# Kernel tuning notes

Hardware: AMD Instinct MI355X
Metric: run time of the kernel (lower is better)

## Reference

```python
import jax, jax.numpy as jnp
import numpy as np

WINDOW = (2, 7, 7)
DIM = 128
HEADS = 4
N = WINDOW[0] * WINDOW[1] * WINDOW[2]  # 98
TABLE = (2 * WINDOW[0] - 1) * (2 * WINDOW[1] - 1) * (2 * WINDOW[2] - 1)  # 507


def _rel_pos_index():
    d, h, w = WINDOW
    coords = np.stack(np.meshgrid(np.arange(d), np.arange(h), np.arange(w), indexing='ij'))  # [3,d,h,w]
    cf = coords.reshape(3, -1)  # [3, N]
    rel = cf[:, :, None] - cf[:, None, :]  # [3, N, N]
    rel = rel.transpose(1, 2, 0).copy()
    rel[:, :, 0] += d - 1
    rel[:, :, 1] += h - 1
    rel[:, :, 2] += w - 1
    rel[:, :, 0] *= (2 * h - 1) * (2 * w - 1)
    rel[:, :, 1] *= 2 * w - 1
    return jnp.asarray(rel.sum(-1), dtype=jnp.int32)  # [N, N]

REL_IDX = _rel_pos_index()


def setup_inputs() -> dict:
    key = jax.random.key(0)
    ks = jax.random.split(key, 8)
    B_, nW = 2048, 64
    x = jax.random.normal(ks[0], (B_, N, DIM), dtype=jnp.float32)
    mask = jax.random.normal(ks[1], (nW, N, N), dtype=jnp.float32)
    qkv_w = jax.random.normal(ks[2], (3 * DIM, DIM), dtype=jnp.float32) * (DIM ** -0.5)
    qkv_b = jnp.zeros((3 * DIM,), dtype=jnp.float32)
    rpb_table = jax.random.normal(ks[3], (TABLE, HEADS), dtype=jnp.float32) * 0.02
    proj_w = jax.random.normal(ks[4], (DIM, DIM), dtype=jnp.float32) * (DIM ** -0.5)
    proj_b = jnp.zeros((DIM,), dtype=jnp.float32)
    return {"x": x, "mask": mask, "qkv_w": qkv_w, "qkv_b": qkv_b,
            "rpb_table": rpb_table, "proj_w": proj_w, "proj_b": proj_b}


def reference(x, mask, qkv_w, qkv_b, rpb_table, proj_w, proj_b):
    B_, n, C = x.shape
    hd = C // HEADS
    scale = hd ** -0.5
    qkv = x @ qkv_w.T + qkv_b  # [B_, N, 3C]
    qkv = qkv.reshape(B_, n, 3, HEADS, hd).transpose(2, 0, 3, 1, 4)  # [3, B_, H, N, hd]
    q, k, v = qkv[0], qkv[1], qkv[2]
    attn = jnp.einsum('bhnd,bhmd->bhnm', q * scale, k)  # [B_, H, N, N]
    bias = rpb_table[REL_IDX.reshape(-1)].reshape(n, n, HEADS)  # gather
    attn = attn + bias.transpose(2, 0, 1)[None]  # [B_, H, N, N]
    nW = mask.shape[0]
    attn = attn.reshape(B_ // nW, nW, HEADS, n, n) + mask[None, :, None]
    attn = jax.nn.softmax(attn.reshape(B_, HEADS, n, n), axis=-1)
    out = jnp.einsum('bhnm,bhmd->bhnd', attn, v)  # [B_, H, N, hd]
    out = out.transpose(0, 2, 1, 3).reshape(B_, n, C)
    return out @ proj_w.T + proj_b
```

## Files before the change

kernel.cpp:

```cpp
#include <hip/hip_runtime.h>
#include <hip/hip_bf16.h>

#define NTOK 98
#define CDIM 128
#define SCALE 0.17677669529663687f
#define LOG2E 1.4426950408889634f
#define NEG_BIG -1e30f
#define CMBW 112

typedef short bf16x8 __attribute__((ext_vector_type(8)));
typedef short bf16x4 __attribute__((ext_vector_type(4)));
typedef float f32x4 __attribute__((ext_vector_type(4)));

#define MFMA32(a,b,c) __builtin_amdgcn_mfma_f32_16x16x32_bf16(a,b,c,0,0,0)

#if __has_builtin(__builtin_amdgcn_mfma_f32_16x16x16_bf16)
#define MFMA16(a,b,c) __builtin_amdgcn_mfma_f32_16x16x16_bf16(a,b,c,0,0,0)
#elif __has_builtin(__builtin_amdgcn_mfma_f32_16x16x16bf16_1k)
#define MFMA16(a,b,c) __builtin_amdgcn_mfma_f32_16x16x16bf16_1k(a,b,c,0,0,0)
#else
__device__ __forceinline__ f32x4 mfma16_asm(bf16x4 a, bf16x4 b, f32x4 c) {
  asm("v_mfma_f32_16x16x16_bf16 %0, %1, %2, %0" : "+v"(c) : "v"(a), "v"(b));
  return c;
}
#define MFMA16(a,b,c) mfma16_asm(a,b,c)
#endif

#if __has_builtin(__builtin_amdgcn_exp2f)
#define EXP2F(x) __builtin_amdgcn_exp2f(x)
#else
#define EXP2F(x) exp2f(x)
#endif
#if __has_builtin(__builtin_amdgcn_rcpf)
#define RCPF(x) __builtin_amdgcn_rcpf(x)
#else
#define RCPF(x) (1.f / (x))
#endif

__device__ __forceinline__ unsigned short f2bf(float f) {
  __hip_bfloat16 h = __float2bfloat16(f);
  unsigned short u;
  __builtin_memcpy(&u, &h, 2);
  return u;
}
__device__ __forceinline__ float bf2f(unsigned short b) {
  union { unsigned u; float f; } v; v.u = ((unsigned)b) << 16; return v.f;
}
__device__ __forceinline__ bf16x4 cvt4(f32x4 v) {
  __hip_bfloat162 a = __float22bfloat162_rn(make_float2(v[0], v[1]));
  __hip_bfloat162 b = __float22bfloat162_rn(make_float2(v[2], v[3]));
  bf16x4 r;
  __builtin_memcpy(&r, &a, 4);
  __builtin_memcpy(((char*)&r) + 4, &b, 4);
  return r;
}

__device__ __forceinline__ int swzK(int row, int col) {
  return row * 128 + (col ^ ((row & 7) << 3));
}

__device__ __forceinline__ bf16x8 ldfrag(const float* __restrict__ p) {
  float4 a = *(const float4*)p;
  float4 b = *(const float4*)(p + 4);
  bf16x8 fr;
  fr[0]=(short)f2bf(a.x); fr[1]=(short)f2bf(a.y); fr[2]=(short)f2bf(a.z); fr[3]=(short)f2bf(a.w);
  fr[4]=(short)f2bf(b.x); fr[5]=(short)f2bf(b.y); fr[6]=(short)f2bf(b.z); fr[7]=(short)f2bf(b.w);
  return fr;
}

__device__ __forceinline__ int pcode(int t) {
  int d = t / 49, r = t % 49;
  return d * 169 + (r / 7) * 13 + (r % 7);
}

__global__ __launch_bounds__(512)
void prep_w(const float* __restrict__ qkv_w, const float* __restrict__ qkv_b,
            const float* __restrict__ proj_w, const float* __restrict__ proj_b,
            unsigned short* __restrict__ qpre, unsigned short* __restrict__ ppre,
            float* __restrict__ bpre)
{
  int gid = blockIdx.x * 512 + threadIdx.x;
  if (gid < 6144) {
    int t = gid >> 8, rem = gid & 255, kk = rem >> 6, ln = rem & 63;
    int row = t * 16 + (ln & 15), col = kk * 32 + (ln >> 4) * 8;
    float sc = (row < CDIM) ? SCALE * LOG2E : 1.f;
    const float* s = qkv_w + (size_t)row * CDIM + col;
    unsigned short* d = qpre + (size_t)gid * 8;
#pragma unroll
    for (int e = 0; e < 8; ++e) d[e] = f2bf(s[e] * sc);
  } else if (gid < 8192) {
    int f2 = gid - 6144;
    int t = f2 >> 8, rem = f2 & 255, kk = rem >> 6, ln = rem & 63;
    const float* s = proj_w + (size_t)(t * 16 + (ln & 15)) * CDIM + kk * 32 + (ln >> 4) * 8;
    unsigned short* d = ppre + (size_t)f2 * 8;
#pragma unroll
    for (int e = 0; e < 8; ++e) d[e] = f2bf(s[e]);
  } else {
    int i = gid - 8192;
    if (i < 384) bpre[i] = qkv_b[i] * (i < CDIM ? SCALE * LOG2E : 1.f);
    else if (i < 512) bpre[i] = proj_b[i - 384];
  }
}

__global__ __launch_bounds__(256)
void prep_cmb(const float* __restrict__ mask, const float* __restrict__ rpb,
              float* __restrict__ cmb, int nW)
{
  const int total = 256 * NTOK * CMBW;
  for (int idx = blockIdx.x * 256 + threadIdx.x; idx < total; idx += gridDim.x * 256) {
    int row = idx / CMBW, n = idx - row * CMBW;
    int wh = row / NTOK, m = row - wh * NTOK;
    int w = wh >> 2, h = wh & 3;
    float v = NEG_BIG;
    if (n < NTOK)
      v = (mask[((size_t)w * NTOK + m) * NTOK + n]
           + rpb[(pcode(m) - pcode(n) + 253) * 4 + h]) * LOG2E;
    cmb[idx] = v;
  }
}

template<bool PRE>
__global__ __launch_bounds__(512, 4)
void win_attn(const float* __restrict__ x, const float* __restrict__ mask,
              const float* __restrict__ qkv_w, const float* __restrict__ qkv_b,
              const float* __restrict__ rpb, const float* __restrict__ proj_w,
              const float* __restrict__ proj_b, float* __restrict__ out, int nW,
              const float* __restrict__ cmb, const unsigned short* __restrict__ qpre,
              const unsigned short* __restrict__ ppre, const float* __restrict__ bpre)
{
  __shared__ __align__(16) unsigned short xs[(PRE ? 112 : 98) * 128];
  __shared__ __align__(16) unsigned short kbuf[98 * 128];
  __shared__ __align__(16) unsigned short vbuf[128 * 100];
  __shared__ unsigned short rpbL[PRE ? 2 : 2028];
  __shared__ short mcode[PRE ? 2 : 112];

  const int tid = threadIdx.x;
  const int lane = tid & 63;
  const int wv = tid >> 6;
  const int lm = lane & 15;
  const int lg = lane >> 4;
  const int blk = blockIdx.x;
  const int wmod = blk % nW;
  const float* __restrict__ xblk = x + (size_t)blk * (NTOK * CDIM);
  const float* __restrict__ maskw = mask + (size_t)wmod * (NTOK * NTOK);

  if constexpr (!PRE) {
    if (tid < 112) mcode[tid] = (short)(tid < NTOK ? pcode(tid) : 0);
    for (int i = tid; i < 2028; i += 512) rpbL[i] = f2bf(rpb[i]);
  }
  for (int v = tid; v < NTOK * 32; v += 512) {
    int row = v >> 5, c4 = (v & 31) << 2;
    float4 f = *(const float4*)(xblk + row * CDIM + c4);
    f32x4 fv; fv[0]=f.x; fv[1]=f.y; fv[2]=f.z; fv[3]=f.w;
    *(bf16x4*)&xs[swzK(row, c4)] = cvt4(fv);
  }
  __syncthreads();

  auto wq = [&](int t, int kk) -> bf16x8 {
    if constexpr (PRE) return *(const bf16x8*)&qpre[(size_t)((t * 4 + kk) * 64 + lane) * 8];
    else return ldfrag(qkv_w + (size_t)(t * 16 + lm) * CDIM + kk * 32 + lg * 8);
  };

  {
    bf16x8 Bk[4], Bv[4];
#pragma unroll
    for (int kk = 0; kk < 4; ++kk) { Bk[kk] = wq(8 + wv, kk); Bv[kk] = wq(16 + wv, kk); }
    const float4 bk4 = *(const float4*)((PRE ? bpre : qkv_b) + CDIM + wv * 16 + lg * 4);
    const float  bv_ = (PRE ? bpre : qkv_b)[2 * CDIM + wv * 16 + lm];
    for (int mi = 0; mi < 7; ++mi) {
      int arow = mi * 16 + lm; if (arow > 97) arow = 97;
      bf16x8 A[4];
#pragma unroll
      for (int kk = 0; kk < 4; ++kk) A[kk] = *(const bf16x8*)&xs[swzK(arow, kk * 32 + lg * 8)];
      f32x4 ak = {0.f,0.f,0.f,0.f}, av = {0.f,0.f,0.f,0.f};
#pragma unroll
      for (int kk = 0; kk < 4; ++kk) {
        ak = MFMA32(Bk[kk], A[kk], ak);
        av = MFMA32(A[kk], Bv[kk], av);
      }
      int ktok = mi * 16 + lm;
      if (ktok < NTOK) {
        f32x4 t;
#pragma unroll
        for (int r = 0; r < 4; ++r) t[r] = ak[r] + ((const float*)&bk4)[r];
        *(bf16x4*)&kbuf[swzK(ktok, wv * 16 + lg * 4)] = cvt4(t);
      }
      int vtok0 = mi * 16 + lg * 4;
      if (vtok0 < 100) {
        f32x4 t;
#pragma unroll
        for (int r = 0; r < 4; ++r) t[r] = av[r] + bv_;
        *(bf16x4*)&vbuf[(size_t)(wv * 16 + lm) * 100 + vtok0] = cvt4(t);
      }
    }
  }

  const bool have1 = (wv < 6);
  const int hh0 = wv / 7, mi0 = wv % 7;
  const int mi1 = wv + 1;

  bf16x4 bq[2][2][2];
#pragma unroll
  for (int j = 0; j < 2; ++j) {
    if (j == 0 || have1) {
      const int mi = j ? mi1 : mi0, hh = j ? 1 : hh0;
      int arow = mi * 16 + lm; if (arow > 97) arow = 97;
      bf16x8 Xf[4];
#pragma unroll
      for (int kk = 0; kk < 4; ++kk) Xf[kk] = *(const bf16x8*)&xs[swzK(arow, kk * 32 + lg * 8)];
#pragma unroll
      for (int g = 0; g < 2; ++g) {
        const int h = 2 * g + hh;
#pragma unroll
        for (int ct = 0; ct < 2; ++ct) {
          const int t = h * 2 + ct;
          f32x4 acc = {0.f,0.f,0.f,0.f};
#pragma unroll
          for (int kk = 0; kk < 4; ++kk) acc = MFMA32(wq(t, kk), Xf[kk], acc);
          const float4 qb4 = *(const float4*)((PRE ? bpre : qkv_b) + t * 16 + lg * 4);
          f32x4 tq;
#pragma unroll
          for (int r = 0; r < 4; ++r) {
            float vq = acc[r] + ((const float*)&qb4)[r];
            if constexpr (!PRE) vq *= SCALE * LOG2E;
            tq[r] = vq;
          }
          bq[j][g][ct] = cvt4(tq);
        }
      }
    }
  }
  __syncthreads();

#pragma unroll
  for (int g = 0; g < 2; ++g) {
#pragma unroll
    for (int j = 0; j < 2; ++j) {
      if (j == 0 || have1) {
        const int mi = j ? mi1 : mi0, hh = j ? 1 : hh0;
        const int h = 2 * g + hh, cb = h * 32;
        f32x4 s[7];
        __builtin_amdgcn_s_setprio(1);
#pragma unroll
        for (int nj = 0; nj < 7; ++nj) {
          int krow = nj * 16 + lm; if (krow > 97) krow = 97;
          bf16x4 k0 = *(const bf16x4*)&kbuf[swzK(krow, cb + lg * 4)];
          bf16x4 k1 = *(const bf16x4*)&kbuf[swzK(krow, cb + 16 + lg * 4)];
          f32x4 z = {0.f,0.f,0.f,0.f};
          z = MFMA16(k0, bq[j][g][0], z);
          s[nj] = MFMA16(k1, bq[j][g][1], z);
        }
        __builtin_amdgcn_s_setprio(0);
        const int m = mi * 16 + lm;
        const int mclamp = m > 97 ? 97 : m;
        float sum = 0.f;
        if constexpr (PRE) {
          const float* __restrict__ cp =
              cmb + ((size_t)(wmod * 4 + h) * NTOK + mclamp) * CMBW + lg * 4;
#pragma unroll
          for (int nj = 0; nj < 7; ++nj) {
            float4 cv = *(const float4*)(cp + nj * 16);
#pragma unroll
            for (int r = 0; r < 4; ++r) {
              float e = EXP2F(s[nj][r] + ((const float*)&cv)[r]);
              s[nj][r] = e; sum += e;
            }
          }
        } else {
          const int cm4 = ((int)mcode[mclamp]) * 4 + h + 1012;
          const float* __restrict__ mrow = maskw + mclamp * NTOK;
#pragma unroll
          for (int nj = 0; nj < 7; ++nj) {
            const int n0 = nj * 16 + lg * 4;
#pragma unroll
            for (int r = 0; r < 4; ++r) {
              int n = n0 + r;
              float val = NEG_BIG;
              if (n < NTOK)
                val = s[nj][r] + (mrow[n] + bf2f(rpbL[cm4 - ((int)mcode[n]) * 4])) * LOG2E;
              float e = EXP2F(val);
              s[nj][r] = e; sum += e;
            }
          }
        }
        sum += __shfl_xor(sum, 16);
        sum += __shfl_xor(sum, 32);
        const float inv = RCPF(sum);
        float invr[4];
#pragma unroll
        for (int r = 0; r < 4; ++r) invr[r] = __shfl(inv, lg * 4 + r);
        bf16x4 pp[7];
#pragma unroll
        for (int nj = 0; nj < 7; ++nj) pp[nj] = cvt4(s[nj]);
#pragma unroll
        for (int dt = 0; dt < 2; ++dt) {
          const int d = cb + dt * 16 + lm;
          f32x4 acc = {0.f,0.f,0.f,0.f};
          __builtin_amdgcn_s_setprio(1);
#pragma unroll
          for (int nj = 0; nj < 7; ++nj) {
            const int vc = nj < 6 ? nj * 16 + lg * 4 : 96;
            bf16x4 bv = *(const bf16x4*)&vbuf[(size_t)d * 100 + vc];
            acc = MFMA16(pp[nj], bv, acc);
          }
          __builtin_amdgcn_s_setprio(0);
#pragma unroll
          for (int r = 0; r < 4; ++r) {
            int m2 = mi * 16 + lg * 4 + r;
            if (PRE || m2 < NTOK) xs[swzK(m2, d)] = f2bf(acc[r] * invr[r]);
          }
        }
      }
    }
  }
  __syncthreads();

  {
    bf16x8 Bp[4];
#pragma unroll
    for (int kk = 0; kk < 4; ++kk) {
      if constexpr (PRE) Bp[kk] = *(const bf16x8*)&ppre[(size_t)((wv * 4 + kk) * 64 + lane) * 8];
      else Bp[kk] = ldfrag(proj_w + (size_t)(wv * 16 + lm) * CDIM + kk * 32 + lg * 8);
    }
    const float4 pb4 = *(const float4*)((PRE ? bpre + 384 : proj_b) + wv * 16 + lg * 4);
    float* __restrict__ outb = out + (size_t)blk * (NTOK * CDIM);
    for (int mi = 0; mi < 7; ++mi) {
      int orow = mi * 16 + lm;
      if (!PRE && orow > 97) orow = 97;
      f32x4 acc = {0.f,0.f,0.f,0.f};
#pragma unroll
      for (int kk = 0; kk < 4; ++kk) {
        bf16x8 Bo = *(const bf16x8*)&xs[swzK(orow, kk * 32 + lg * 8)];
        acc = MFMA32(Bp[kk], Bo, acc);
      }
      int tok = mi * 16 + lm;
      if (tok < NTOK) {
        float4 o4;
        o4.x = acc[0] + pb4.x; o4.y = acc[1] + pb4.y;
        o4.z = acc[2] + pb4.z; o4.w = acc[3] + pb4.w;
        *(float4*)(outb + (size_t)tok * CDIM + wv * 16 + lg * 4) = o4;
      }
    }
  }
}

extern "C" void kernel_launch(void* const* d_in, const int* in_sizes, int n_in,
                              void* d_out, int out_size, void* d_ws, size_t ws_size,
                              hipStream_t stream) {
  const float* x      = (const float*)d_in[0];
  const float* mask   = (const float*)d_in[1];
  const float* qkv_w  = (const float*)d_in[2];
  const float* qkv_b  = (const float*)d_in[3];
  const float* rpb    = (const float*)d_in[4];
  const float* proj_w = (const float*)d_in[5];
  const float* proj_b = (const float*)d_in[6];
  int B  = in_sizes[0] / (NTOK * CDIM);
  int nW = in_sizes[1] / (NTOK * NTOK);

  const size_t CMB_B  = (size_t)256 * NTOK * CMBW * 4;
  const size_t QPRE_B = 24 * 4 * 64 * 8 * 2;
  const size_t PPRE_B = 8 * 4 * 64 * 8 * 2;
  const size_t BIAS_B = 512 * 4;
  const size_t need = CMB_B + QPRE_B + PPRE_B + BIAS_B;

  if (ws_size >= need) {
    float* cmb = (float*)d_ws;
    unsigned short* qpre = (unsigned short*)((char*)d_ws + CMB_B);
    unsigned short* ppre = (unsigned short*)((char*)d_ws + CMB_B + QPRE_B);
    float* bpre = (float*)((char*)d_ws + CMB_B + QPRE_B + PPRE_B);
    hipLaunchKernelGGL(prep_w, dim3(17), dim3(512), 0, stream,
                       qkv_w, qkv_b, proj_w, proj_b, qpre, ppre, bpre);
    hipLaunchKernelGGL(prep_cmb, dim3(1024), dim3(256), 0, stream, mask, rpb, cmb, nW);
    hipLaunchKernelGGL(win_attn<true>, dim3(B), dim3(512), 0, stream,
                       x, mask, qkv_w, qkv_b, rpb, proj_w, proj_b, (float*)d_out, nW,
                       cmb, qpre, ppre, bpre);
  } else {
    hipLaunchKernelGGL(win_attn<false>, dim3(B), dim3(512), 0, stream,
                       x, mask, qkv_w, qkv_b, rpb, proj_w, proj_b, (float*)d_out, nW,
                       (const float*)nullptr, (const unsigned short*)nullptr,
                       (const unsigned short*)nullptr, (const float*)nullptr);
  }
}
```

Before: 138.0 us.

## Double block to 1024 threads and redistribute K/V, attention and proj work across 16 waves

Launches each window block with 16 waves instead of 8. Waves 0-7 compute K and waves 8-15 compute V, and each of 14 waves now owns one (head-pair, row-tile) attention task instead of two. The output projection is split so each column tile is handled by two waves over separate row ranges. The aim is to shorten each block's serial critical path and give the scheduler more waves to hide latency. The cost is a tighter per-thread register budget under launch_bounds(1024, 8), with possible spills, and two idle waves during attention.

```diff
diff --git a/kernel.cpp b/kernel.cpp
--- a/kernel.cpp
+++ b/kernel.cpp
@@ -120,7 +120,7 @@
 }
 
 template<bool PRE>
-__global__ __launch_bounds__(512, 4)
+__global__ __launch_bounds__(1024, 8)
 void win_attn(const float* __restrict__ x, const float* __restrict__ mask,
               const float* __restrict__ qkv_w, const float* __restrict__ qkv_b,
               const float* __restrict__ rpb, const float* __restrict__ proj_w,
@@ -143,12 +143,13 @@
   const int wmod = blk % nW;
   const float* __restrict__ xblk = x + (size_t)blk * (NTOK * CDIM);
   const float* __restrict__ maskw = mask + (size_t)wmod * (NTOK * NTOK);
+  const float* __restrict__ bias = PRE ? bpre : qkv_b;
 
   if constexpr (!PRE) {
     if (tid < 112) mcode[tid] = (short)(tid < NTOK ? pcode(tid) : 0);
-    for (int i = tid; i < 2028; i += 512) rpbL[i] = f2bf(rpb[i]);
-  }
-  for (int v = tid; v < NTOK * 32; v += 512) {
+    for (int i = tid; i < 2028; i += 1024) rpbL[i] = f2bf(rpb[i]);
+  }
+  for (int v = tid; v < NTOK * 32; v += 1024) {
     int row = v >> 5, c4 = (v & 31) << 2;
     float4 f = *(const float4*)(xblk + row * CDIM + c4);
     f32x4 fv; fv[0]=f.x; fv[1]=f.y; fv[2]=f.z; fv[3]=f.w;
@@ -161,23 +162,19 @@
     else return ldfrag(qkv_w + (size_t)(t * 16 + lm) * CDIM + kk * 32 + lg * 8);
   };
 
-  {
-    bf16x8 Bk[4], Bv[4];
-#pragma unroll
-    for (int kk = 0; kk < 4; ++kk) { Bk[kk] = wq(8 + wv, kk); Bv[kk] = wq(16 + wv, kk); }
-    const float4 bk4 = *(const float4*)((PRE ? bpre : qkv_b) + CDIM + wv * 16 + lg * 4);
-    const float  bv_ = (PRE ? bpre : qkv_b)[2 * CDIM + wv * 16 + lm];
+  if (wv < 8) {
+    bf16x8 Bk[4];
+#pragma unroll
+    for (int kk = 0; kk < 4; ++kk) Bk[kk] = wq(8 + wv, kk);
+    const float4 bk4 = *(const float4*)(bias + CDIM + wv * 16 + lg * 4);
     for (int mi = 0; mi < 7; ++mi) {
       int arow = mi * 16 + lm; if (arow > 97) arow = 97;
       bf16x8 A[4];
 #pragma unroll
       for (int kk = 0; kk < 4; ++kk) A[kk] = *(const bf16x8*)&xs[swzK(arow, kk * 32 + lg * 8)];
-      f32x4 ak = {0.f,0.f,0.f,0.f}, av = {0.f,0.f,0.f,0.f};
-#pragma unroll
-      for (int kk = 0; kk < 4; ++kk) {
-        ak = MFMA32(Bk[kk], A[kk], ak);
-        av = MFMA32(A[kk], Bv[kk], av);
-      }
+      f32x4 ak = {0.f,0.f,0.f,0.f};
+#pragma unroll
+      for (int kk = 0; kk < 4; ++kk) ak = MFMA32(Bk[kk], A[kk], ak);
       int ktok = mi * 16 + lm;
       if (ktok < NTOK) {
         f32x4 t;
@@ -185,147 +182,155 @@
         for (int r = 0; r < 4; ++r) t[r] = ak[r] + ((const float*)&bk4)[r];
         *(bf16x4*)&kbuf[swzK(ktok, wv * 16 + lg * 4)] = cvt4(t);
       }
+    }
+  } else {
+    const int vt = wv - 8;
+    bf16x8 Bv[4];
+#pragma unroll
+    for (int kk = 0; kk < 4; ++kk) Bv[kk] = wq(16 + vt, kk);
+    const float bv_ = bias[2 * CDIM + vt * 16 + lm];
+    for (int mi = 0; mi < 7; ++mi) {
+      int arow = mi * 16 + lm; if (arow > 97) arow = 97;
+      bf16x8 A[4];
+#pragma unroll
+      for (int kk = 0; kk < 4; ++kk) A[kk] = *(const bf16x8*)&xs[swzK(arow, kk * 32 + lg * 8)];
+      f32x4 av = {0.f,0.f,0.f,0.f};
+#pragma unroll
+      for (int kk = 0; kk < 4; ++kk) av = MFMA32(A[kk], Bv[kk], av);
       int vtok0 = mi * 16 + lg * 4;
       if (vtok0 < 100) {
         f32x4 t;
 #pragma unroll
         for (int r = 0; r < 4; ++r) t[r] = av[r] + bv_;
-        *(bf16x4*)&vbuf[(size_t)(wv * 16 + lm) * 100 + vtok0] = cvt4(t);
-      }
-    }
-  }
-
-  const bool have1 = (wv < 6);
-  const int hh0 = wv / 7, mi0 = wv % 7;
-  const int mi1 = wv + 1;
-
-  bf16x4 bq[2][2][2];
-#pragma unroll
-  for (int j = 0; j < 2; ++j) {
-    if (j == 0 || have1) {
-      const int mi = j ? mi1 : mi0, hh = j ? 1 : hh0;
-      int arow = mi * 16 + lm; if (arow > 97) arow = 97;
-      bf16x8 Xf[4];
-#pragma unroll
-      for (int kk = 0; kk < 4; ++kk) Xf[kk] = *(const bf16x8*)&xs[swzK(arow, kk * 32 + lg * 8)];
-#pragma unroll
-      for (int g = 0; g < 2; ++g) {
-        const int h = 2 * g + hh;
-#pragma unroll
-        for (int ct = 0; ct < 2; ++ct) {
-          const int t = h * 2 + ct;
-          f32x4 acc = {0.f,0.f,0.f,0.f};
-#pragma unroll
-          for (int kk = 0; kk < 4; ++kk) acc = MFMA32(wq(t, kk), Xf[kk], acc);
-          const float4 qb4 = *(const float4*)((PRE ? bpre : qkv_b) + t * 16 + lg * 4);
-          f32x4 tq;
+        *(bf16x4*)&vbuf[(size_t)(vt * 16 + lm) * 100 + vtok0] = cvt4(t);
+      }
+    }
+  }
+
+  const bool active = (wv < 14);
+  const int hh = wv / 7, mi = wv % 7;
+
+  bf16x4 bq[2][2];
+  if (active) {
+    int arow = mi * 16 + lm; if (arow > 97) arow = 97;
+    bf16x8 Xf[4];
+#pragma unroll
+    for (int kk = 0; kk < 4; ++kk) Xf[kk] = *(const bf16x8*)&xs[swzK(arow, kk * 32 + lg * 8)];
+#pragma unroll
+    for (int g = 0; g < 2; ++g) {
+      const int h = 2 * g + hh;
+#pragma unroll
+      for (int ct = 0; ct < 2; ++ct) {
+        const int t = h * 2 + ct;
+        f32x4 acc = {0.f,0.f,0.f,0.f};
+#pragma unroll
+        for (int kk = 0; kk < 4; ++kk) acc = MFMA32(wq(t, kk), Xf[kk], acc);
+        const float4 qb4 = *(const float4*)(bias + t * 16 + lg * 4);
+        f32x4 tq;
+#pragma unroll
+        for (int r = 0; r < 4; ++r) {
+          float vq = acc[r] + ((const float*)&qb4)[r];
+          if constexpr (!PRE) vq *= SCALE * LOG2E;
+          tq[r] = vq;
+        }
+        bq[g][ct] = cvt4(tq);
+      }
+    }
+  }
+  __syncthreads();
+
+#pragma unroll
+  for (int g = 0; g < 2; ++g) {
+    if (active) {
+      const int h = 2 * g + hh, cb = h * 32;
+      f32x4 s[7];
+      __builtin_amdgcn_s_setprio(1);
+#pragma unroll
+      for (int nj = 0; nj < 7; ++nj) {
+        int krow = nj * 16 + lm; if (krow > 97) krow = 97;
+        bf16x4 k0 = *(const bf16x4*)&kbuf[swzK(krow, cb + lg * 4)];
+        bf16x4 k1 = *(const bf16x4*)&kbuf[swzK(krow, cb + 16 + lg * 4)];
+        f32x4 z = {0.f,0.f,0.f,0.f};
+        z = MFMA16(k0, bq[g][0], z);
+        s[nj] = MFMA16(k1, bq[g][1], z);
+      }
+      __builtin_amdgcn_s_setprio(0);
+      const int m = mi * 16 + lm;
+      const int mclamp = m > 97 ? 97 : m;
+      float sum = 0.f;
+      if constexpr (PRE) {
+        const float* __restrict__ cp =
+            cmb + ((size_t)(wmod * 4 + h) * NTOK + mclamp) * CMBW + lg * 4;
+#pragma unroll
+        for (int nj = 0; nj < 7; ++nj) {
+          float4 cv = *(const float4*)(cp + nj * 16);
 #pragma unroll
           for (int r = 0; r < 4; ++r) {
-            float vq = acc[r] + ((const float*)&qb4)[r];
-            if constexpr (!PRE) vq *= SCALE * LOG2E;
-            tq[r] = vq;
+            float e = EXP2F(s[nj][r] + ((const float*)&cv)[r]);
+            s[nj][r] = e; sum += e;
           }
-          bq[j][g][ct] = cvt4(tq);
+        }
+      } else {
+        const int cm4 = ((int)mcode[mclamp]) * 4 + h + 1012;
+        const float* __restrict__ mrow = maskw + mclamp * NTOK;
+#pragma unroll
+        for (int nj = 0; nj < 7; ++nj) {
+          const int n0 = nj * 16 + lg * 4;
+#pragma unroll
+          for (int r = 0; r < 4; ++r) {
+            int n = n0 + r;
+            float val = NEG_BIG;
+            if (n < NTOK)
+              val = s[nj][r] + (mrow[n] + bf2f(rpbL[cm4 - ((int)mcode[n]) * 4])) * LOG2E;
+            float e = EXP2F(val);
+            s[nj][r] = e; sum += e;
+          }
+        }
+      }
+      sum += __shfl_xor(sum, 16);
+      sum += __shfl_xor(sum, 32);
+      const float inv = RCPF(sum);
+      float invr[4];
+#pragma unroll
+      for (int r = 0; r < 4; ++r) invr[r] = __shfl(inv, lg * 4 + r);
+      bf16x4 pp[7];
+#pragma unroll
+      for (int nj = 0; nj < 7; ++nj) pp[nj] = cvt4(s[nj]);
+#pragma unroll
+      for (int dt = 0; dt < 2; ++dt) {
+        const int d = cb + dt * 16 + lm;
+        f32x4 acc = {0.f,0.f,0.f,0.f};
+        __builtin_amdgcn_s_setprio(1);
+#pragma unroll
+        for (int nj = 0; nj < 7; ++nj) {
+          const int vc = nj < 6 ? nj * 16 + lg * 4 : 96;
+          bf16x4 bv = *(const bf16x4*)&vbuf[(size_t)d * 100 + vc];
+          acc = MFMA16(pp[nj], bv, acc);
+        }
+        __builtin_amdgcn_s_setprio(0);
+#pragma unroll
+        for (int r = 0; r < 4; ++r) {
+          int m2 = mi * 16 + lg * 4 + r;
+          if (PRE || m2 < NTOK) xs[swzK(m2, d)] = f2bf(acc[r] * invr[r]);
         }
       }
     }
   }
   __syncthreads();
 
-#pragma unroll
-  for (int g = 0; g < 2; ++g) {
-#pragma unroll
-    for (int j = 0; j < 2; ++j) {
-      if (j == 0 || have1) {
-        const int mi = j ? mi1 : mi0, hh = j ? 1 : hh0;
-        const int h = 2 * g + hh, cb = h * 32;
-        f32x4 s[7];
-        __builtin_amdgcn_s_setprio(1);
-#pragma unroll
-        for (int nj = 0; nj < 7; ++nj) {
-          int krow = nj * 16 + lm; if (krow > 97) krow = 97;
-          bf16x4 k0 = *(const bf16x4*)&kbuf[swzK(krow, cb + lg * 4)];
-          bf16x4 k1 = *(const bf16x4*)&kbuf[swzK(krow, cb + 16 + lg * 4)];
-          f32x4 z = {0.f,0.f,0.f,0.f};
-          z = MFMA16(k0, bq[j][g][0], z);
-          s[nj] = MFMA16(k1, bq[j][g][1], z);
-        }
-        __builtin_amdgcn_s_setprio(0);
-        const int m = mi * 16 + lm;
-        const int mclamp = m > 97 ? 97 : m;
-        float sum = 0.f;
-        if constexpr (PRE) {
-          const float* __restrict__ cp =
-              cmb + ((size_t)(wmod * 4 + h) * NTOK + mclamp) * CMBW + lg * 4;
-#pragma unroll
-          for (int nj = 0; nj < 7; ++nj) {
-            float4 cv = *(const float4*)(cp + nj * 16);
-#pragma unroll
-            for (int r = 0; r < 4; ++r) {
-              float e = EXP2F(s[nj][r] + ((const float*)&cv)[r]);
-              s[nj][r] = e; sum += e;
-            }
-          }
-        } else {
-          const int cm4 = ((int)mcode[mclamp]) * 4 + h + 1012;
-          const float* __restrict__ mrow = maskw + mclamp * NTOK;
-#pragma unroll
-          for (int nj = 0; nj < 7; ++nj) {
-            const int n0 = nj * 16 + lg * 4;
-#pragma unroll
-            for (int r = 0; r < 4; ++r) {
-              int n = n0 + r;
-              float val = NEG_BIG;
-              if (n < NTOK)
-                val = s[nj][r] + (mrow[n] + bf2f(rpbL[cm4 - ((int)mcode[n]) * 4])) * LOG2E;
-              float e = EXP2F(val);
-              s[nj][r] = e; sum += e;
-            }
-          }
-        }
-        sum += __shfl_xor(sum, 16);
-        sum += __shfl_xor(sum, 32);
-        const float inv = RCPF(sum);
-        float invr[4];
-#pragma unroll
-        for (int r = 0; r < 4; ++r) invr[r] = __shfl(inv, lg * 4 + r);
-        bf16x4 pp[7];
-#pragma unroll
-        for (int nj = 0; nj < 7; ++nj) pp[nj] = cvt4(s[nj]);
-#pragma unroll
-        for (int dt = 0; dt < 2; ++dt) {
-          const int d = cb + dt * 16 + lm;
-          f32x4 acc = {0.f,0.f,0.f,0.f};
-          __builtin_amdgcn_s_setprio(1);
-#pragma unroll
-          for (int nj = 0; nj < 7; ++nj) {
-            const int vc = nj < 6 ? nj * 16 + lg * 4 : 96;
-            bf16x4 bv = *(const bf16x4*)&vbuf[(size_t)d * 100 + vc];
-            acc = MFMA16(pp[nj], bv, acc);
-          }
-          __builtin_amdgcn_s_setprio(0);
-#pragma unroll
-          for (int r = 0; r < 4; ++r) {
-            int m2 = mi * 16 + lg * 4 + r;
-            if (PRE || m2 < NTOK) xs[swzK(m2, d)] = f2bf(acc[r] * invr[r]);
-          }
-        }
-      }
-    }
-  }
-  __syncthreads();
-
   {
+    const int ct8 = wv & 7;
     bf16x8 Bp[4];
 #pragma unroll
     for (int kk = 0; kk < 4; ++kk) {
-      if constexpr (PRE) Bp[kk] = *(const bf16x8*)&ppre[(size_t)((wv * 4 + kk) * 64 + lane) * 8];
-      else Bp[kk] = ldfrag(proj_w + (size_t)(wv * 16 + lm) * CDIM + kk * 32 + lg * 8);
-    }
-    const float4 pb4 = *(const float4*)((PRE ? bpre + 384 : proj_b) + wv * 16 + lg * 4);
+      if constexpr (PRE) Bp[kk] = *(const bf16x8*)&ppre[(size_t)((ct8 * 4 + kk) * 64 + lane) * 8];
+      else Bp[kk] = ldfrag(proj_w + (size_t)(ct8 * 16 + lm) * CDIM + kk * 32 + lg * 8);
+    }
+    const float4 pb4 = *(const float4*)((PRE ? bpre + 384 : proj_b) + ct8 * 16 + lg * 4);
     float* __restrict__ outb = out + (size_t)blk * (NTOK * CDIM);
-    for (int mi = 0; mi < 7; ++mi) {
-      int orow = mi * 16 + lm;
+    const int mlo = wv < 8 ? 0 : 4, mhi = wv < 8 ? 4 : 7;
+    for (int mi2 = mlo; mi2 < mhi; ++mi2) {
+      int orow = mi2 * 16 + lm;
       if (!PRE && orow > 97) orow = 97;
       f32x4 acc = {0.f,0.f,0.f,0.f};
 #pragma unroll
@@ -333,12 +338,12 @@
         bf16x8 Bo = *(const bf16x8*)&xs[swzK(orow, kk * 32 + lg * 8)];
         acc = MFMA32(Bp[kk], Bo, acc);
       }
-      int tok = mi * 16 + lm;
+      int tok = mi2 * 16 + lm;
       if (tok < NTOK) {
         float4 o4;
         o4.x = acc[0] + pb4.x; o4.y = acc[1] + pb4.y;
         o4.z = acc[2] + pb4.z; o4.w = acc[3] + pb4.w;
-        *(float4*)(outb + (size_t)tok * CDIM + wv * 16 + lg * 4) = o4;
+        *(float4*)(outb + (size_t)tok * CDIM + ct8 * 16 + lg * 4) = o4;
       }
     }
   }
@@ -371,11 +376,11 @@
     hipLaunchKernelGGL(prep_w, dim3(17), dim3(512), 0, stream,
                        qkv_w, qkv_b, proj_w, proj_b, qpre, ppre, bpre);
     hipLaunchKernelGGL(prep_cmb, dim3(1024), dim3(256), 0, stream, mask, rpb, cmb, nW);
-    hipLaunchKernelGGL(win_attn<true>, dim3(B), dim3(512), 0, stream,
+    hipLaunchKernelGGL(win_attn<true>, dim3(B), dim3(1024), 0, stream,
                        x, mask, qkv_w, qkv_b, rpb, proj_w, proj_b, (float*)d_out, nW,
                        cmb, qpre, ppre, bpre);
   } else {
-    hipLaunchKernelGGL(win_attn<false>, dim3(B), dim3(512), 0, stream,
+    hipLaunchKernelGGL(win_attn<false>, dim3(B), dim3(1024), 0, stream,
                        x, mask, qkv_w, qkv_b, rpb, proj_w, proj_b, (float*)d_out, nW,
                        (const float*)nullptr, (const unsigned short*)nullptr,
                        (const unsigned short*)nullptr, (const float*)nullptr);
```

Measured after the change: 127.0 us. 1.09x faster.
